# Performance work log

Hardware: AMD Instinct MI355X
Metric: run time of the kernel (lower is better)

## Reference

```python
import jax, jax.numpy as jnp
import numpy as np

NUM_HEADS = 16
HEAD_DIM = 128
ROT_DIM = 128  # rotary_emb_dim == head_dim
ROPE_BASE = 10000.0


def setup_inputs() -> dict:
    key = jax.random.key(0)
    k1, k2, k3, k4, k5 = jax.random.split(key, 5)
    b, s, d = 2, 2048, 2048
    return {
        "x": jax.random.normal(k1, (b, s, d), jnp.float32),
        "Wqkv_w": jax.random.normal(k2, (3 * d, d), jnp.float32) * (d ** -0.5),
        "Wqkv_b": jax.random.normal(k3, (3 * d,), jnp.float32) * 0.02,
        "wo_w": jax.random.normal(k4, (d, d), jnp.float32) * (d ** -0.5),
        "wo_b": jax.random.normal(k5, (d,), jnp.float32) * 0.02,
    }


def _deinterleave(t):
    # torch.cat([t[..., ::2], t[..., 1::2]], dim=-1)
    return jnp.concatenate([t[..., ::2], t[..., 1::2]], axis=-1)


def _rope(t, cos, sin):
    # non-interleaved (GPT-NeoX style) rotary on first ROT_DIM dims; here ROT_DIM == head_dim
    half = ROT_DIM // 2
    x1, x2 = t[..., :half], t[..., half:ROT_DIM]
    # cos/sin: (s, half) -> broadcast over (b, s, h, half)
    c = cos[None, :, None, :]
    sn = sin[None, :, None, :]
    return jnp.concatenate([x1 * c - x2 * sn, x2 * c + x1 * sn], axis=-1)


def reference(x, Wqkv_w, Wqkv_b, wo_w, wo_b):
    b, s, d = x.shape
    h, hd = NUM_HEADS, HEAD_DIM
    # fused QKV projection, layout '(h three d)' per original rearrange
    qkv = x @ Wqkv_w.T + Wqkv_b                      # (b, s, 3*d)
    qkv = qkv.reshape(b, s, h, 3, hd)
    q = _deinterleave(qkv[:, :, :, 0, :])            # (b, s, h, hd)
    k = _deinterleave(qkv[:, :, :, 1, :])
    v = qkv[:, :, :, 2, :]
    # rotary embedding tables
    inv_freq = 1.0 / (ROPE_BASE ** (jnp.arange(0, ROT_DIM, 2, dtype=jnp.float32) / ROT_DIM))
    freqs = jnp.arange(s, dtype=jnp.float32)[:, None] * inv_freq[None, :]  # (s, half)
    cos, sin = jnp.cos(freqs), jnp.sin(freqs)
    q = _rope(q, cos, sin)
    k = _rope(k, cos, sin)
    # causal self-attention (SelfAttention, softmax_scale = 1/sqrt(hd))
    scale = hd ** -0.5
    scores = jnp.einsum('bshd,bthd->bhst', q, k) * scale  # (b, h, s, s)
    mask = jnp.tril(jnp.ones((s, s), dtype=bool))
    scores = jnp.where(mask[None, None], scores, jnp.finfo(scores.dtype).min)
    probs = jax.nn.softmax(scores, axis=-1)
    ctx = jnp.einsum('bhst,bthd->bshd', probs, v)    # (b, s, h, hd)
    ctx = ctx.reshape(b, s, d)
    return ctx @ wo_w.T + wo_b
```

## Files before the change

### kernel.cpp

```cpp
#include <hip/hip_runtime.h>

#define B_ 2
#define S_ 2048
#define H_ 16
#define HD_ 128
#define QKVROW 6144
#define M_ 4096

typedef float f32x4 __attribute__((ext_vector_type(4)));
typedef __bf16 bf16x8 __attribute__((ext_vector_type(8)));
typedef unsigned short ushortx8 __attribute__((ext_vector_type(8)));

__device__ __forceinline__ float bf2f(unsigned short u) {
  union { unsigned u; float f; } v;
  v.u = ((unsigned)u) << 16;
  return v.f;
}
__device__ __forceinline__ unsigned short f2bf(float f) {
  union { __bf16 b; unsigned short u; } c;
  c.b = (__bf16)f;
  return c.u;
}
__device__ __forceinline__ ushortx8 cvt8(const float* f) {
  const f32x4 lo = *(const f32x4*)f;
  const f32x4 hi = *(const f32x4*)(f + 4);
  ushortx8 o;
#pragma unroll
  for (int t = 0; t < 4; ++t) o[t] = f2bf(lo[t]);
#pragma unroll
  for (int t = 0; t < 4; ++t) o[4 + t] = f2bf(hi[t]);
  return o;
}
__device__ __forceinline__ void async16(const unsigned short* g, unsigned short* l) {
  __builtin_amdgcn_global_load_lds(
      (const __attribute__((address_space(1))) unsigned int*)g,
      (__attribute__((address_space(3))) unsigned int*)l, 16, 0, 0);
}

__global__ __launch_bounds__(256) void rope_table(float* __restrict__ tab) {
  const int i = blockIdx.x * 256 + threadIdx.x;
  const int s = i >> 6, t = i & 63;
  const float invf = expf(-(float)t * 0.14391156831212787f);
  float sn, cs;
  sincosf((float)s * invf, &sn, &cs);
  tab[2 * i] = cs;
  tab[2 * i + 1] = sn;
}

__global__ __launch_bounds__(256) void f2bf3(
    const float* __restrict__ a, unsigned short* __restrict__ da, int na8,
    const float* __restrict__ b, unsigned short* __restrict__ db, int nb8,
    const float* __restrict__ c, unsigned short* __restrict__ dc, int nc8) {
  const int ntot = na8 + nb8 + nc8;
  int i = blockIdx.x * 256 + threadIdx.x;
  const int stride = gridDim.x * 256;
  for (; i < ntot; i += stride) {
    const float* s;
    unsigned short* d;
    int off = i;
    if (off < na8) { s = a; d = da; }
    else if (off - na8 < nb8) { off -= na8; s = b; d = db; }
    else { off -= na8 + nb8; s = c; d = dc; }
    const ushortx8 o = cvt8(s + (size_t)off * 8);
    *(ushortx8*)&d[(size_t)off * 8] = o;
  }
}

__global__ __launch_bounds__(256) void gemm1(
    const unsigned short* __restrict__ A, const unsigned short* __restrict__ Bm,
    const float* __restrict__ bias, unsigned short* __restrict__ C) {
  __shared__ unsigned short As[128 * 64];
  __shared__ unsigned short Bs[128 * 64];
  const int tid = threadIdx.x;
  const int lane = tid & 63, wave = tid >> 6;
  const int l15 = lane & 15, quad = lane >> 4;
  const int m0 = blockIdx.y * 128, n0 = blockIdx.x * 128;
  const int wr = (wave >> 1) * 64, wc = (wave & 1) * 64;

  f32x4 acc[4][4];
#pragma unroll
  for (int r = 0; r < 4; ++r)
#pragma unroll
    for (int c = 0; c < 4; ++c) acc[r][c] = (f32x4){0.f, 0.f, 0.f, 0.f};

  for (int k0 = 0; k0 < 2048; k0 += 64) {
    __syncthreads();
#pragma unroll
    for (int i = 0; i < 4; ++i) {
      const int c0 = wave * 256 + i * 64;
      const int u = c0 + lane;
      const int row = u >> 3, cu = u & 7;
      const int cs = cu ^ (row & 7);
      async16(A + (size_t)(m0 + row) * 2048 + k0 + cs * 8, &As[c0 * 8]);
      async16(Bm + (size_t)(n0 + row) * 2048 + k0 + cs * 8, &Bs[c0 * 8]);
    }
    __syncthreads();

#pragma unroll
    for (int s = 0; s < 2; ++s) {
      bf16x8 af[4], bf[4];
#pragma unroll
      for (int r = 0; r < 4; ++r) {
        const int row = wr + r * 16 + l15;
        af[r] = *(const bf16x8*)&As[row * 64 + (((s * 4 + quad) ^ (row & 7)) << 3)];
      }
#pragma unroll
      for (int c = 0; c < 4; ++c) {
        const int row = wc + c * 16 + l15;
        bf[c] = *(const bf16x8*)&Bs[row * 64 + (((s * 4 + quad) ^ (row & 7)) << 3)];
      }
#pragma unroll
      for (int r = 0; r < 4; ++r)
#pragma unroll
        for (int c = 0; c < 4; ++c)
          acc[r][c] = __builtin_amdgcn_mfma_f32_16x16x32_bf16(af[r], bf[c], acc[r][c], 0, 0, 0);
    }
  }

#pragma unroll
  for (int c = 0; c < 4; ++c) {
    const int col = n0 + wc + c * 16 + l15;
    const float bv = bias[col];
#pragma unroll
    for (int r = 0; r < 4; ++r) {
      const int row = m0 + wr + r * 16 + quad * 4;
#pragma unroll
      for (int i = 0; i < 4; ++i)
        C[(size_t)(row + i) * QKVROW + col] = f2bf(acc[r][c][i] + bv);
    }
  }
}

__global__ __launch_bounds__(256) void rope_vt(
    unsigned short* qkv, unsigned short* __restrict__ Vt,
    const float* __restrict__ tab) {
  __shared__ unsigned short vs[64 * 136];
  const int b = blockIdx.z, h = blockIdx.y, s0 = blockIdx.x * 64;
  const int tid = threadIdx.x;
  const int r = tid >> 2, cpart = (tid & 3) * 32;
  const int s = s0 + r;
  unsigned short* base = qkv + (size_t)(b * S_ + s) * QKVROW + h * 384;
  const int j0 = cpart >> 1;

  ushortx8 ivq[4], ivk[4], ivv[4];
#pragma unroll
  for (int i = 0; i < 4; ++i) {
    ivq[i] = *(const ushortx8*)&base[cpart + i * 8];
    ivk[i] = *(const ushortx8*)&base[128 + cpart + i * 8];
    ivv[i] = *(const ushortx8*)&base[256 + cpart + i * 8];
  }

  float cs[16], sn[16];
  {
    const f32x4* tr = (const f32x4*)&tab[(size_t)s * 128 + j0 * 2];
#pragma unroll
    for (int t = 0; t < 8; ++t) {
      const f32x4 v = tr[t];
      cs[2 * t] = v[0]; sn[2 * t] = v[1];
      cs[2 * t + 1] = v[2]; sn[2 * t + 1] = v[3];
    }
  }

  __syncthreads();

#pragma unroll
  for (int which = 0; which < 2; ++which) {
    const ushortx8* iv = (which == 0) ? ivq : ivk;
    const float scale = (which == 0) ? 0.08838834764831845f : 1.0f;
    ushortx8 o1a, o1b, o2a, o2b;
#pragma unroll
    for (int t = 0; t < 16; ++t) {
      const float x1 = bf2f(iv[(2 * t) >> 3][(2 * t) & 7]);
      const float x2 = bf2f(iv[(2 * t + 1) >> 3][(2 * t + 1) & 7]);
      const unsigned short r1 = f2bf((x1 * cs[t] - x2 * sn[t]) * scale);
      const unsigned short r2 = f2bf((x2 * cs[t] + x1 * sn[t]) * scale);
      if (t < 8) { o1a[t] = r1; o2a[t] = r2; }
      else       { o1b[t - 8] = r1; o2b[t - 8] = r2; }
    }
    unsigned short* out = base + which * 128;
    *(ushortx8*)&out[j0] = o1a;
    *(ushortx8*)&out[j0 + 8] = o1b;
    *(ushortx8*)&out[64 + j0] = o2a;
    *(ushortx8*)&out[64 + j0 + 8] = o2b;
  }

#pragma unroll
  for (int i = 0; i < 4; ++i)
    *(ushortx8*)&vs[r * 136 + cpart + i * 8] = ivv[i];
  __syncthreads();
  const size_t vtb = (size_t)(b * H_ + h) * HD_ * S_ + s0;
#pragma unroll
  for (int it = 0; it < 4; ++it) {
    const int a = tid + it * 256;
    const int d = a >> 3, sc = (a & 7) * 8;
    ushortx8 o;
#pragma unroll
    for (int t = 0; t < 8; ++t) o[t] = vs[(sc + t) * 136 + d];
    *(ushortx8*)&Vt[vtb + (size_t)d * S_ + sc] = o;
  }
}

__global__ __launch_bounds__(512) void attn(
    unsigned short* qkv, const unsigned short* __restrict__ Vt) {
  __shared__ unsigned short Ks[64 * 136];
  __shared__ unsigned short Vs[128 * 72];
  __shared__ unsigned short Ps[8 * 16 * 72];
  const int p = blockIdx.x, bh = blockIdx.y;
  const int b = bh >> 4, h = bh & 15;
  const int tid = threadIdx.x, lane = tid & 63, wave = tid >> 6;
  const int l15 = lane & 15, quad = lane >> 4;

  unsigned short* qh = qkv + (size_t)b * S_ * QKVROW + h * 384;
  const unsigned short* Vb = Vt + (size_t)bh * HD_ * S_;
  unsigned short* Pw = &Ps[wave * 16 * 72];

  ushortx8 rk[2], rv[2];
  auto pref = [&](int j) {
#pragma unroll
    for (int t = 0; t < 2; ++t) {
      const int uk = t * 512 + tid;
      const int krow = uk >> 4, kcu = uk & 15;
      rk[t] = *(const ushortx8*)(qh + (size_t)(j * 64 + krow) * QKVROW + 128 + kcu * 8);
      const int vrow = uk >> 3, vcu = uk & 7;
      rv[t] = *(const ushortx8*)(Vb + (size_t)vrow * S_ + j * 64 + vcu * 8);
    }
  };
  pref(0);

#pragma unroll
  for (int half = 0; half < 2; ++half) {
    const int qt = half ? 15 - p : p;
    const int jN = 2 * qt + 2;

    bf16x8 aq[4];
#pragma unroll
    for (int ks = 0; ks < 4; ++ks)
      aq[ks] = *(const bf16x8*)&qh[(size_t)(qt * 128 + wave * 16 + l15) * QKVROW +
                                   ks * 32 + quad * 8];

    f32x4 o[8];
    float mrow[4], lrow[4];
#pragma unroll
    for (int ct = 0; ct < 8; ++ct) o[ct] = (f32x4){0.f, 0.f, 0.f, 0.f};
#pragma unroll
    for (int i = 0; i < 4; ++i) { mrow[i] = -1e30f; lrow[i] = 0.f; }

    for (int j = 0; j < jN; ++j) {
      __syncthreads();
#pragma unroll
      for (int t = 0; t < 2; ++t) {
        const int uk = t * 512 + tid;
        *(ushortx8*)&Ks[(uk >> 4) * 136 + (uk & 15) * 8] = rk[t];
        *(ushortx8*)&Vs[(uk >> 3) * 72 + (uk & 7) * 8] = rv[t];
      }
      __syncthreads();

      const int jn = (j + 1 < jN) ? j + 1 : (half == 0 ? 0 : -1);
      if (jn >= 0) pref(jn);

      f32x4 sacc[4];
#pragma unroll
      for (int ct = 0; ct < 4; ++ct) sacc[ct] = (f32x4){0.f, 0.f, 0.f, 0.f};
#pragma unroll
      for (int ks = 0; ks < 4; ++ks) {
        bf16x8 bk[4];
#pragma unroll
        for (int ct = 0; ct < 4; ++ct)
          bk[ct] = *(const bf16x8*)&Ks[(ct * 16 + l15) * 136 + ks * 32 + quad * 8];
#pragma unroll
        for (int ct = 0; ct < 4; ++ct)
          sacc[ct] = __builtin_amdgcn_mfma_f32_16x16x32_bf16(aq[ks], bk[ct], sacc[ct], 0, 0, 0);
      }

      if (j >= 2 * qt) {
#pragma unroll
        for (int ct = 0; ct < 4; ++ct)
#pragma unroll
          for (int i = 0; i < 4; ++i) {
            const int grow = qt * 128 + wave * 16 + quad * 4 + i;
            const int gcol = j * 64 + ct * 16 + l15;
            if (gcol > grow) sacc[ct][i] = -1e30f;
          }
      }

#pragma unroll
      for (int i = 0; i < 4; ++i) {
        float m = sacc[0][i];
#pragma unroll
        for (int ct = 1; ct < 4; ++ct) m = fmaxf(m, sacc[ct][i]);
#pragma unroll
        for (int off = 1; off < 16; off <<= 1) m = fmaxf(m, __shfl_xor(m, off));
        const float mn = fmaxf(mrow[i], m);
        const float alpha = __expf(mrow[i] - mn);
        mrow[i] = mn;
        float rsum = 0.f;
#pragma unroll
        for (int ct = 0; ct < 4; ++ct) {
          const float pv = __expf(sacc[ct][i] - mn);
          sacc[ct][i] = pv;
          rsum += pv;
        }
#pragma unroll
        for (int off = 1; off < 16; off <<= 1) rsum += __shfl_xor(rsum, off);
        lrow[i] = lrow[i] * alpha + rsum;
#pragma unroll
        for (int ct = 0; ct < 8; ++ct) o[ct][i] *= alpha;
      }

#pragma unroll
      for (int ct = 0; ct < 4; ++ct)
#pragma unroll
        for (int i = 0; i < 4; ++i)
          Pw[(quad * 4 + i) * 72 + ct * 16 + l15] = f2bf(sacc[ct][i]);

#pragma unroll
      for (int ks = 0; ks < 2; ++ks) {
        const bf16x8 ap = *(const bf16x8*)&Pw[l15 * 72 + ks * 32 + quad * 8];
        bf16x8 bv[8];
#pragma unroll
        for (int ct = 0; ct < 8; ++ct)
          bv[ct] = *(const bf16x8*)&Vs[(ct * 16 + l15) * 72 + ks * 32 + quad * 8];
#pragma unroll
        for (int ct = 0; ct < 8; ++ct)
          o[ct] = __builtin_amdgcn_mfma_f32_16x16x32_bf16(ap, bv[ct], o[ct], 0, 0, 0);
      }
    }

    float inv[4];
#pragma unroll
    for (int i = 0; i < 4; ++i) inv[i] = 1.0f / lrow[i];
#pragma unroll
    for (int ct = 0; ct < 8; ++ct)
#pragma unroll
      for (int i = 0; i < 4; ++i) {
        const int srow = qt * 128 + wave * 16 + quad * 4 + i;
        qh[(size_t)srow * QKVROW + ct * 16 + l15] = f2bf(o[ct][i] * inv[i]);
      }
  }
}

__global__ __launch_bounds__(256) void gemm2(
    const unsigned short* __restrict__ A, const unsigned short* __restrict__ Bm,
    const float* __restrict__ bias, float* __restrict__ C) {
  __shared__ unsigned short As[128 * 64];
  __shared__ unsigned short Bs[128 * 64];
  const int tid = threadIdx.x;
  const int lane = tid & 63, wave = tid >> 6;
  const int l15 = lane & 15, quad = lane >> 4;
  const int m0 = blockIdx.y * 128, n0 = blockIdx.x * 128;
  const int wr = (wave >> 1) * 64, wc = (wave & 1) * 64;

  f32x4 acc[4][4];
#pragma unroll
  for (int r = 0; r < 4; ++r)
#pragma unroll
    for (int c = 0; c < 4; ++c) acc[r][c] = (f32x4){0.f, 0.f, 0.f, 0.f};

  for (int k0 = 0; k0 < 2048; k0 += 64) {
    const int kh = ((k0 >> 7) * 384) + (k0 & 127);
    __syncthreads();
#pragma unroll
    for (int i = 0; i < 4; ++i) {
      const int c0 = wave * 256 + i * 64;
      const int u = c0 + lane;
      const int row = u >> 3, cu = u & 7;
      const int cs = cu ^ (row & 7);
      async16(A + (size_t)(m0 + row) * QKVROW + kh + cs * 8, &As[c0 * 8]);
      async16(Bm + (size_t)(n0 + row) * 2048 + k0 + cs * 8, &Bs[c0 * 8]);
    }
    __syncthreads();

#pragma unroll
    for (int s = 0; s < 2; ++s) {
      bf16x8 af[4], bf[4];
#pragma unroll
      for (int r = 0; r < 4; ++r) {
        const int row = wr + r * 16 + l15;
        af[r] = *(const bf16x8*)&As[row * 64 + (((s * 4 + quad) ^ (row & 7)) << 3)];
      }
#pragma unroll
      for (int c = 0; c < 4; ++c) {
        const int row = wc + c * 16 + l15;
        bf[c] = *(const bf16x8*)&Bs[row * 64 + (((s * 4 + quad) ^ (row & 7)) << 3)];
      }
#pragma unroll
      for (int r = 0; r < 4; ++r)
#pragma unroll
        for (int c = 0; c < 4; ++c)
          acc[r][c] = __builtin_amdgcn_mfma_f32_16x16x32_bf16(af[r], bf[c], acc[r][c], 0, 0, 0);
    }
  }

#pragma unroll
  for (int c = 0; c < 4; ++c) {
    const int col = n0 + wc + c * 16 + l15;
    const float bv = bias[col];
#pragma unroll
    for (int r = 0; r < 4; ++r) {
      const int row = m0 + wr + r * 16 + quad * 4;
#pragma unroll
      for (int i = 0; i < 4; ++i)
        C[(size_t)(row + i) * 2048 + col] = acc[r][c][i] + bv;
    }
  }
}

extern "C" void kernel_launch(void* const* d_in, const int* in_sizes, int n_in,
                              void* d_out, int out_size, void* d_ws, size_t ws_size,
                              hipStream_t stream) {
  const float* x    = (const float*)d_in[0];
  const float* wqkv = (const float*)d_in[1];
  const float* bqkv = (const float*)d_in[2];
  const float* wo   = (const float*)d_in[3];
  const float* bo   = (const float*)d_in[4];
  float* out = (float*)d_out;

  unsigned short* qkv = (unsigned short*)d_ws;
  unsigned short* Vt  = qkv + (size_t)M_ * QKVROW;
  unsigned short* xb  = Vt  + (size_t)B_ * H_ * HD_ * S_;
  unsigned short* wb  = xb  + (size_t)M_ * 2048;
  unsigned short* wob = wb  + (size_t)QKVROW * 2048;
  float* tab = (float*)(wob + (size_t)2048 * 2048);

  rope_table<<<dim3((S_ * 64) / 256), 256, 0, stream>>>(tab);
  f2bf3<<<dim3(2048), 256, 0, stream>>>(x, xb, (M_ * 2048) / 8,
                                        wqkv, wb, (QKVROW * 2048) / 8,
                                        wo, wob, (2048 * 2048) / 8);

  gemm1<<<dim3(QKVROW / 128, M_ / 128), 256, 0, stream>>>(xb, wb, bqkv, qkv);
  rope_vt<<<dim3(S_ / 64, H_, B_), 256, 0, stream>>>(qkv, Vt, tab);
  attn<<<dim3(8, B_ * H_), 512, 0, stream>>>(qkv, Vt);
  gemm2<<<dim3(2048 / 128, M_ / 128), 256, 0, stream>>>(qkv, wob, bo, out);
}
```

Before: 412.4 us.

## Double-buffer LDS tiles in QKV and output GEMMs with async prefetch

```diff
diff --git a/kernel.cpp b/kernel.cpp
--- a/kernel.cpp
+++ b/kernel.cpp
@@ -69,8 +69,8 @@
 __global__ __launch_bounds__(256) void gemm1(
     const unsigned short* __restrict__ A, const unsigned short* __restrict__ Bm,
     const float* __restrict__ bias, unsigned short* __restrict__ C) {
-  __shared__ unsigned short As[128 * 64];
-  __shared__ unsigned short Bs[128 * 64];
+  __shared__ unsigned short As[2][128 * 64];
+  __shared__ unsigned short Bs[2][128 * 64];
   const int tid = threadIdx.x;
   const int lane = tid & 63, wave = tid >> 6;
   const int l15 = lane & 15, quad = lane >> 4;
@@ -83,18 +83,27 @@
 #pragma unroll
     for (int c = 0; c < 4; ++c) acc[r][c] = (f32x4){0.f, 0.f, 0.f, 0.f};
 
-  for (int k0 = 0; k0 < 2048; k0 += 64) {
-    __syncthreads();
+  auto stage = [&](int t, int b) {
 #pragma unroll
     for (int i = 0; i < 4; ++i) {
       const int c0 = wave * 256 + i * 64;
       const int u = c0 + lane;
       const int row = u >> 3, cu = u & 7;
       const int cs = cu ^ (row & 7);
-      async16(A + (size_t)(m0 + row) * 2048 + k0 + cs * 8, &As[c0 * 8]);
-      async16(Bm + (size_t)(n0 + row) * 2048 + k0 + cs * 8, &Bs[c0 * 8]);
-    }
-    __syncthreads();
+      async16(A + (size_t)(m0 + row) * 2048 + t * 64 + cs * 8, &As[b][c0 * 8]);
+      async16(Bm + (size_t)(n0 + row) * 2048 + t * 64 + cs * 8, &Bs[b][c0 * 8]);
+    }
+  };
+
+  stage(0, 0);
+  stage(1, 1);
+
+  for (int kt = 0; kt < 32; ++kt) {
+    const int b = kt & 1;
+    if (kt < 31) asm volatile("s_waitcnt vmcnt(8)" ::: "memory");
+    else         asm volatile("s_waitcnt vmcnt(0)" ::: "memory");
+    __builtin_amdgcn_s_barrier();
+    __builtin_amdgcn_sched_barrier(0);
 
 #pragma unroll
     for (int s = 0; s < 2; ++s) {
@@ -102,12 +111,12 @@
 #pragma unroll
       for (int r = 0; r < 4; ++r) {
         const int row = wr + r * 16 + l15;
-        af[r] = *(const bf16x8*)&As[row * 64 + (((s * 4 + quad) ^ (row & 7)) << 3)];
+        af[r] = *(const bf16x8*)&As[b][row * 64 + (((s * 4 + quad) ^ (row & 7)) << 3)];
       }
 #pragma unroll
       for (int c = 0; c < 4; ++c) {
         const int row = wc + c * 16 + l15;
-        bf[c] = *(const bf16x8*)&Bs[row * 64 + (((s * 4 + quad) ^ (row & 7)) << 3)];
+        bf[c] = *(const bf16x8*)&Bs[b][row * 64 + (((s * 4 + quad) ^ (row & 7)) << 3)];
       }
 #pragma unroll
       for (int r = 0; r < 4; ++r)
@@ -115,6 +124,12 @@
         for (int c = 0; c < 4; ++c)
           acc[r][c] = __builtin_amdgcn_mfma_f32_16x16x32_bf16(af[r], bf[c], acc[r][c], 0, 0, 0);
     }
+
+    asm volatile("s_waitcnt lgkmcnt(0)" ::: "memory");
+    __builtin_amdgcn_sched_barrier(0);
+    __builtin_amdgcn_s_barrier();
+    __builtin_amdgcn_sched_barrier(0);
+    if (kt + 2 < 32) stage(kt + 2, b);
   }
 
 #pragma unroll
@@ -342,8 +357,8 @@
 __global__ __launch_bounds__(256) void gemm2(
     const unsigned short* __restrict__ A, const unsigned short* __restrict__ Bm,
     const float* __restrict__ bias, float* __restrict__ C) {
-  __shared__ unsigned short As[128 * 64];
-  __shared__ unsigned short Bs[128 * 64];
+  __shared__ unsigned short As[2][128 * 64];
+  __shared__ unsigned short Bs[2][128 * 64];
   const int tid = threadIdx.x;
   const int lane = tid & 63, wave = tid >> 6;
   const int l15 = lane & 15, quad = lane >> 4;
@@ -356,19 +371,29 @@
 #pragma unroll
     for (int c = 0; c < 4; ++c) acc[r][c] = (f32x4){0.f, 0.f, 0.f, 0.f};
 
-  for (int k0 = 0; k0 < 2048; k0 += 64) {
+  auto stage = [&](int t, int b) {
+    const int k0 = t * 64;
     const int kh = ((k0 >> 7) * 384) + (k0 & 127);
-    __syncthreads();
 #pragma unroll
     for (int i = 0; i < 4; ++i) {
       const int c0 = wave * 256 + i * 64;
       const int u = c0 + lane;
       const int row = u >> 3, cu = u & 7;
       const int cs = cu ^ (row & 7);
-      async16(A + (size_t)(m0 + row) * QKVROW + kh + cs * 8, &As[c0 * 8]);
-      async16(Bm + (size_t)(n0 + row) * 2048 + k0 + cs * 8, &Bs[c0 * 8]);
-    }
-    __syncthreads();
+      async16(A + (size_t)(m0 + row) * QKVROW + kh + cs * 8, &As[b][c0 * 8]);
+      async16(Bm + (size_t)(n0 + row) * 2048 + k0 + cs * 8, &Bs[b][c0 * 8]);
+    }
+  };
+
+  stage(0, 0);
+  stage(1, 1);
+
+  for (int kt = 0; kt < 32; ++kt) {
+    const int b = kt & 1;
+    if (kt < 31) asm volatile("s_waitcnt vmcnt(8)" ::: "memory");
+    else         asm volatile("s_waitcnt vmcnt(0)" ::: "memory");
+    __builtin_amdgcn_s_barrier();
+    __builtin_amdgcn_sched_barrier(0);
 
 #pragma unroll
     for (int s = 0; s < 2; ++s) {
@@ -376,12 +401,12 @@
 #pragma unroll
       for (int r = 0; r < 4; ++r) {
         const int row = wr + r * 16 + l15;
-        af[r] = *(const bf16x8*)&As[row * 64 + (((s * 4 + quad) ^ (row & 7)) << 3)];
+        af[r] = *(const bf16x8*)&As[b][row * 64 + (((s * 4 + quad) ^ (row & 7)) << 3)];
       }
 #pragma unroll
       for (int c = 0; c < 4; ++c) {
         const int row = wc + c * 16 + l15;
-        bf[c] = *(const bf16x8*)&Bs[row * 64 + (((s * 4 + quad) ^ (row & 7)) << 3)];
+        bf[c] = *(const bf16x8*)&Bs[b][row * 64 + (((s * 4 + quad) ^ (row & 7)) << 3)];
       }
 #pragma unroll
       for (int r = 0; r < 4; ++r)
@@ -389,6 +414,12 @@
         for (int c = 0; c < 4; ++c)
           acc[r][c] = __builtin_amdgcn_mfma_f32_16x16x32_bf16(af[r], bf[c], acc[r][c], 0, 0, 0);
     }
+
+    asm volatile("s_waitcnt lgkmcnt(0)" ::: "memory");
+    __builtin_amdgcn_sched_barrier(0);
+    __builtin_amdgcn_s_barrier();
+    __builtin_amdgcn_sched_barrier(0);
+    if (kt + 2 < 32) stage(kt + 2, b);
   }
 
 #pragma unroll
```

Result: no change. 419.3 us (+1.7%).
